# Kernel tuning notes

Measured on AMD Instinct MI355X. Metric: run time of the kernel, lower is better.

## Reference

```python
import jax, jax.numpy as jnp
import numpy as np

B, T, H, DFF = 32, 4096, 512, 512  # hidden_size=512, d_ff=512, h feature dim = 2*H


def setup_inputs() -> dict:
    key = jax.random.key(0)
    ks = jax.random.split(key, 8)
    sc = 0.02
    return {
        "s": jax.random.normal(ks[0], (B, H), dtype=jnp.float32),
        "h": jax.random.normal(ks[1], (B, T, 2 * H), dtype=jnp.float32),
        "W_a_w": jax.random.normal(ks[2], (DFF, H), dtype=jnp.float32) * sc,
        "W_a_b": jnp.zeros((DFF,), dtype=jnp.float32),
        "U_a_w": jax.random.normal(ks[3], (DFF, 2 * H), dtype=jnp.float32) * sc,
        "U_a_b": jnp.zeros((DFF,), dtype=jnp.float32),
        "V_a_w": jax.random.normal(ks[4], (1, DFF), dtype=jnp.float32) * sc,
        "V_a_b": jnp.zeros((1,), dtype=jnp.float32),
    }


def reference(s, h, W_a_w, W_a_b, U_a_w, U_a_b, V_a_w, V_a_b):
    # Bahdanau additive attention scoring (NOTE: original has no softmax).
    ws = s @ W_a_w.T + W_a_b                              # [B, d_ff]
    uh = jnp.einsum('bte,fe->btf', h, U_a_w) + U_a_b       # [B, T, d_ff]
    x = jnp.tanh(ws[:, None, :] + uh)                      # [B, T, d_ff]
    energy = x @ V_a_w[0] + V_a_b[0]                       # [B, T]
    context = jnp.einsum('bt,bte->be', energy, h)          # [B, 2*hidden]
    return context
```

## Files before the change

### kernel.cpp

```cpp
#include <hip/hip_runtime.h>
#include <cstdint>
#include <cstddef>

#define B_SZ 32
#define T_SZ 4096
#define H2   1024
#define DFF_ 512
#define TM   64
#define BK   32
#define SPH  16
#define NSTEP 32

typedef __attribute__((ext_vector_type(8))) short bf16x8;
typedef __attribute__((ext_vector_type(4))) float f32x4;

__device__ __forceinline__ unsigned short f2bf(float x) {
  unsigned u = __float_as_uint(x);
  u += 0x7fffu + ((u >> 16) & 1u);
  return (unsigned short)(u >> 16);
}

__global__ void prep_u_kernel(const float* __restrict__ U,
                              unsigned short* __restrict__ Upk) {
  int g = blockIdx.x * 256 + threadIdx.x;
  int j  = g & 7;
  int l  = (g >> 3) & 63;
  int ct = (g >> 9) & 31;
  int ks = g >> 14;
  int f  = ct * 16 + (l & 15);
  int k  = ks * 32 + (l >> 4) * 8 + j;
  Upk[g] = f2bf(U[f * H2 + k]);
}

__global__ void prep_ws_kernel(const float* __restrict__ s, const float* __restrict__ W,
                               const float* __restrict__ Wb, const float* __restrict__ Ub,
                               float* __restrict__ wsm) {
  int idx = blockIdx.x * 256 + threadIdx.x;
  int b = idx >> 9, f = idx & 511;
  const float4* s4 = (const float4*)(s + b * 512);
  const float4* w4 = (const float4*)(W + f * 512);
  float acc = 0.f;
  #pragma unroll 4
  for (int i = 0; i < 128; ++i) {
    float4 a = s4[i], w = w4[i];
    acc += a.x * w.x + a.y * w.y + a.z * w.z + a.w * w.w;
  }
  wsm[idx] = acc + Wb[f] + Ub[f];
}

__global__ __launch_bounds__(512, 4) void attn_main(
    const float* __restrict__ h, const unsigned short* __restrict__ Upk,
    const float* __restrict__ wsm, const float* __restrict__ Vw,
    const float* __restrict__ Vb, float* __restrict__ out) {
  __shared__ unsigned short As[SPH * 2048];
  __shared__ float ws_s[DFF_];
  __shared__ float V_s[DFF_];
  __shared__ float energy_part[8][TM];
  __shared__ float energy_s[TM];

  const int tid  = threadIdx.x;
  const int blk  = blockIdx.x;
  const int b    = blk >> 6;
  const int t0   = (blk & 63) * TM;
  const int lane = tid & 63;
  const int cg   = tid >> 6;
  const int ln15 = lane & 15;
  const int q4   = lane >> 4;

  ws_s[tid] = wsm[b * DFF_ + tid];
  V_s[tid]  = Vw[tid];

  const int arow = tid >> 3;
  const int ak   = (tid & 7) * 4;
  const int a_off = (arow >> 4) * 512 + (ak >> 3) * 128 + (arow & 15) * 8 + (ak & 7);
  const float* hbase = h + ((size_t)(b * T_SZ + t0)) * H2;
  const float* hrow  = hbase + (size_t)arow * H2 + ak;

  const bf16x8* Upk8 = (const bf16x8*)Upk;

  f32x4 acc[16];
  #pragma unroll
  for (int i = 0; i < 16; ++i) acc[i] = (f32x4){0.f, 0.f, 0.f, 0.f};

  for (int hk = 0; hk < 2; ++hk) {
    if (hk) __syncthreads();
    {
      float4 avv[8];
      #pragma unroll
      for (int j = 0; j < 8; ++j) avv[j] = *(const float4*)(hrow + hk * 512 + j * BK);
      #pragma unroll
      for (int j = 0; j < 8; ++j) {
        ushort4 ab;
        ab.x = f2bf(avv[j].x); ab.y = f2bf(avv[j].y);
        ab.z = f2bf(avv[j].z); ab.w = f2bf(avv[j].w);
        *(ushort4*)&As[j * 2048 + a_off] = ab;
      }
      #pragma unroll
      for (int j = 0; j < 8; ++j) avv[j] = *(const float4*)(hrow + hk * 512 + (j + 8) * BK);
      #pragma unroll
      for (int j = 0; j < 8; ++j) {
        ushort4 ab;
        ab.x = f2bf(avv[j].x); ab.y = f2bf(avv[j].y);
        ab.z = f2bf(avv[j].z); ab.w = f2bf(avv[j].w);
        *(ushort4*)&As[(j + 8) * 2048 + a_off] = ab;
      }
    }
    __syncthreads();
    const int ksbase = hk * SPH;
    bf16x8 bcur[4], bnxt[4];
    {
      size_t base = ((size_t)(ksbase * 32 + cg * 4)) * 64 + lane;
      #pragma unroll
      for (int i = 0; i < 4; ++i) bcur[i] = Upk8[base + (size_t)i * 64];
    }
    #pragma unroll
    for (int s = 0; s < SPH; ++s) {
      if (s < SPH - 1) {
        size_t base = ((size_t)((ksbase + s + 1) * 32 + cg * 4)) * 64 + lane;
        #pragma unroll
        for (int i = 0; i < 4; ++i) bnxt[i] = Upk8[base + (size_t)i * 64];
      }
      bf16x8 af[4];
      #pragma unroll
      for (int rt = 0; rt < 4; ++rt)
        af[rt] = *(const bf16x8*)&As[s * 2048 + rt * 512 + lane * 8];
      #pragma unroll
      for (int ct2 = 0; ct2 < 4; ++ct2)
        #pragma unroll
        for (int rt = 0; rt < 4; ++rt)
          acc[ct2 * 4 + rt] =
            __builtin_amdgcn_mfma_f32_16x16x32_bf16(af[rt], bcur[ct2], acc[ct2 * 4 + rt], 0, 0, 0);
      #pragma unroll
      for (int i = 0; i < 4; ++i) bcur[i] = bnxt[i];
    }
  }

  float esum[16];
  #pragma unroll
  for (int i = 0; i < 16; ++i) esum[i] = 0.f;
  #pragma unroll
  for (int ct2 = 0; ct2 < 4; ++ct2) {
    int f = cg * 64 + ct2 * 16 + ln15;
    float wsf = ws_s[f], vf = V_s[f];
    #pragma unroll
    for (int rt = 0; rt < 4; ++rt) {
      #pragma unroll
      for (int rg = 0; rg < 4; ++rg) {
        float z = wsf + acc[ct2 * 4 + rt][rg];
        float e = __expf(2.f * z);
        float x = 1.f - 2.f / (e + 1.f);
        esum[rt * 4 + rg] += x * vf;
      }
    }
  }
  #pragma unroll
  for (int i = 0; i < 16; ++i) {
    #pragma unroll
    for (int m = 1; m < 16; m <<= 1) esum[i] += __shfl_xor(esum[i], m, 64);
  }
  if (ln15 == 0) {
    #pragma unroll
    for (int rt = 0; rt < 4; ++rt)
      #pragma unroll
      for (int rg = 0; rg < 4; ++rg)
        energy_part[cg][rt * 16 + q4 * 4 + rg] = esum[rt * 4 + rg];
  }
  __syncthreads();
  if (tid < TM) {
    float e = Vb[0];
    #pragma unroll
    for (int w = 0; w < 8; ++w) e += energy_part[w][tid];
    energy_s[tid] = e;
  }
  __syncthreads();

  int e0 = tid * 2;
  float c0 = 0.f, c1 = 0.f;
  const float2* h2p = (const float2*)hbase + (e0 >> 1);
  #pragma unroll 4
  for (int row = 0; row < TM; ++row) {
    float en = energy_s[row];
    float2 hv = h2p[(size_t)row * (H2 / 2)];
    c0 += en * hv.x;
    c1 += en * hv.y;
  }
  atomicAdd(&out[b * H2 + e0], c0);
  atomicAdd(&out[b * H2 + e0 + 1], c1);
}

extern "C" void kernel_launch(void* const* d_in, const int* in_sizes, int n_in,
                              void* d_out, int out_size, void* d_ws, size_t ws_size,
                              hipStream_t stream) {
  const float* s  = (const float*)d_in[0];
  const float* h  = (const float*)d_in[1];
  const float* Ww = (const float*)d_in[2];
  const float* Wb = (const float*)d_in[3];
  const float* Uw = (const float*)d_in[4];
  const float* Ub = (const float*)d_in[5];
  const float* Vw = (const float*)d_in[6];
  const float* Vb = (const float*)d_in[7];
  float* out = (float*)d_out;

  unsigned short* Upk = (unsigned short*)d_ws;
  float* wsm = (float*)((char*)d_ws + (size_t)NSTEP * 32768);

  hipMemsetAsync(out, 0, (size_t)out_size * sizeof(float), stream);
  prep_u_kernel<<<(DFF_ * H2) / 256, 256, 0, stream>>>(Uw, Upk);
  prep_ws_kernel<<<(B_SZ * DFF_) / 256, 256, 0, stream>>>(s, Ww, Wb, Ub, wsm);
  attn_main<<<B_SZ * (T_SZ / TM), 512, 0, stream>>>(h, Upk, wsm, Vw, Vb, out);
}
```

Measured before the change: 884.6 us.

## Stream h tiles via async global-to-LDS loads with double-buffered bf16 chunks

Replaces the two large register-staged loads of the h tile with 128-column chunks fetched by global_load_lds directly into an fp32 LDS staging buffer. Each chunk is converted to bf16 in a double-buffered A tile while the next chunk's load is in flight, overlapping memory traffic with MFMA work. LDS use changes: the bf16 A buffer shrinks and an fp32 staging buffer is added, which may alter occupancy, and each chunk adds two more barriers. The context loop unroll is also raised from 4 to 8.

```diff
diff --git a/kernel.cpp b/kernel.cpp
--- a/kernel.cpp
+++ b/kernel.cpp
@@ -7,8 +7,8 @@
 #define H2   1024
 #define DFF_ 512
 #define TM   64
-#define BK   32
-#define SPH  16
+#define CH_K 128
+#define NCHUNK 8
 #define NSTEP 32
 
 typedef __attribute__((ext_vector_type(8))) short bf16x8;
@@ -18,6 +18,12 @@
   unsigned u = __float_as_uint(x);
   u += 0x7fffu + ((u >> 16) & 1u);
   return (unsigned short)(u >> 16);
+}
+
+__device__ __forceinline__ void gll16(const float* g, void* l) {
+  __builtin_amdgcn_global_load_lds(
+      (const __attribute__((address_space(1))) unsigned int*)g,
+      (__attribute__((address_space(3))) unsigned int*)l, 16, 0, 0);
 }
 
 __global__ void prep_u_kernel(const float* __restrict__ U,
@@ -52,7 +58,8 @@
     const float* __restrict__ h, const unsigned short* __restrict__ Upk,
     const float* __restrict__ wsm, const float* __restrict__ Vw,
     const float* __restrict__ Vb, float* __restrict__ out) {
-  __shared__ unsigned short As[SPH * 2048];
+  __shared__ float F32c[8320];
+  __shared__ unsigned short As16[2][4 * 2048];
   __shared__ float ws_s[DFF_];
   __shared__ float V_s[DFF_];
   __shared__ float energy_part[8][TM];
@@ -70,11 +77,15 @@
   ws_s[tid] = wsm[b * DFF_ + tid];
   V_s[tid]  = Vw[tid];
 
-  const int arow = tid >> 3;
-  const int ak   = (tid & 7) * 4;
-  const int a_off = (arow >> 4) * 512 + (ak >> 3) * 128 + (arow & 15) * 8 + (ak & 7);
   const float* hbase = h + ((size_t)(b * T_SZ + t0)) * H2;
-  const float* hrow  = hbase + (size_t)arow * H2 + ak;
+
+  const float* gA = hbase + (size_t)(8 * cg + (lane >> 5)) * H2 + (lane & 31) * 4;
+  char* lA = (char*)F32c + cg * (4 * 1040);
+
+  const int arow  = tid >> 3;
+  const int acq   = tid & 7;
+  const int rbyte = (arow >> 1) * 1040 + (arow & 1) * 512 + acq * 16;
+  const int a_off = (arow >> 4) * 512 + (acq >> 1) * 128 + (arow & 15) * 8 + (acq & 1) * 4;
 
   const bf16x8* Upk8 = (const bf16x8*)Upk;
 
@@ -82,48 +93,55 @@
   #pragma unroll
   for (int i = 0; i < 16; ++i) acc[i] = (f32x4){0.f, 0.f, 0.f, 0.f};
 
-  for (int hk = 0; hk < 2; ++hk) {
-    if (hk) __syncthreads();
-    {
-      float4 avv[8];
-      #pragma unroll
-      for (int j = 0; j < 8; ++j) avv[j] = *(const float4*)(hrow + hk * 512 + j * BK);
-      #pragma unroll
-      for (int j = 0; j < 8; ++j) {
-        ushort4 ab;
-        ab.x = f2bf(avv[j].x); ab.y = f2bf(avv[j].y);
-        ab.z = f2bf(avv[j].z); ab.w = f2bf(avv[j].w);
-        *(ushort4*)&As[j * 2048 + a_off] = ab;
-      }
-      #pragma unroll
-      for (int j = 0; j < 8; ++j) avv[j] = *(const float4*)(hrow + hk * 512 + (j + 8) * BK);
-      #pragma unroll
-      for (int j = 0; j < 8; ++j) {
-        ushort4 ab;
-        ab.x = f2bf(avv[j].x); ab.y = f2bf(avv[j].y);
-        ab.z = f2bf(avv[j].z); ab.w = f2bf(avv[j].w);
-        *(ushort4*)&As[(j + 8) * 2048 + a_off] = ab;
-      }
-    }
-    __syncthreads();
-    const int ksbase = hk * SPH;
-    bf16x8 bcur[4], bnxt[4];
-    {
-      size_t base = ((size_t)(ksbase * 32 + cg * 4)) * 64 + lane;
-      #pragma unroll
-      for (int i = 0; i < 4; ++i) bcur[i] = Upk8[base + (size_t)i * 64];
-    }
-    #pragma unroll
-    for (int s = 0; s < SPH; ++s) {
-      if (s < SPH - 1) {
-        size_t base = ((size_t)((ksbase + s + 1) * 32 + cg * 4)) * 64 + lane;
+  {
+    const float* g0 = gA;
+    gll16(g0,          lA);
+    gll16(g0 + 2 * H2, lA + 1040);
+    gll16(g0 + 4 * H2, lA + 2080);
+    gll16(g0 + 6 * H2, lA + 3120);
+  }
+  asm volatile("s_waitcnt vmcnt(0)" ::: "memory");
+  __syncthreads();
+  {
+    unsigned short* dst = &As16[0][0];
+    #pragma unroll
+    for (int j = 0; j < 4; ++j) {
+      float4 v = *(const float4*)((const char*)F32c + rbyte + j * 128);
+      ushort4 ab;
+      ab.x = f2bf(v.x); ab.y = f2bf(v.y); ab.z = f2bf(v.z); ab.w = f2bf(v.w);
+      *(ushort4*)&dst[j * 2048 + a_off] = ab;
+    }
+  }
+  __syncthreads();
+  {
+    const float* g0 = gA + CH_K;
+    gll16(g0,          lA);
+    gll16(g0 + 2 * H2, lA + 1040);
+    gll16(g0 + 4 * H2, lA + 2080);
+    gll16(g0 + 6 * H2, lA + 3120);
+  }
+
+  bf16x8 bcur[4], bnxt[4];
+  {
+    int ub = (cg * 4) * 64 + lane;
+    #pragma unroll
+    for (int i = 0; i < 4; ++i) bcur[i] = Upk8[ub + i * 64];
+  }
+
+  for (int c2 = 0; c2 < NCHUNK; ++c2) {
+    const unsigned short* Ab = &As16[c2 & 1][0];
+    #pragma unroll
+    for (int sl = 0; sl < 4; ++sl) {
+      if (sl < 3 || c2 < NCHUNK - 1) {
+        int sgn = c2 * 4 + sl + 1;
+        int ub = (sgn * 32 + cg * 4) * 64 + lane;
         #pragma unroll
-        for (int i = 0; i < 4; ++i) bnxt[i] = Upk8[base + (size_t)i * 64];
+        for (int i = 0; i < 4; ++i) bnxt[i] = Upk8[ub + i * 64];
       }
       bf16x8 af[4];
       #pragma unroll
       for (int rt = 0; rt < 4; ++rt)
-        af[rt] = *(const bf16x8*)&As[s * 2048 + rt * 512 + lane * 8];
+        af[rt] = *(const bf16x8*)&Ab[sl * 2048 + rt * 512 + lane * 8];
       #pragma unroll
       for (int ct2 = 0; ct2 < 4; ++ct2)
         #pragma unroll
@@ -133,6 +151,26 @@
       #pragma unroll
       for (int i = 0; i < 4; ++i) bcur[i] = bnxt[i];
     }
+    if (c2 < NCHUNK - 1) {
+      asm volatile("s_waitcnt vmcnt(0)" ::: "memory");
+      __syncthreads();
+      unsigned short* dst = &As16[(c2 + 1) & 1][0];
+      #pragma unroll
+      for (int j = 0; j < 4; ++j) {
+        float4 v = *(const float4*)((const char*)F32c + rbyte + j * 128);
+        ushort4 ab;
+        ab.x = f2bf(v.x); ab.y = f2bf(v.y); ab.z = f2bf(v.z); ab.w = f2bf(v.w);
+        *(ushort4*)&dst[j * 2048 + a_off] = ab;
+      }
+      __syncthreads();
+      if (c2 < NCHUNK - 2) {
+        const float* g0 = gA + (c2 + 2) * CH_K;
+        gll16(g0,          lA);
+        gll16(g0 + 2 * H2, lA + 1040);
+        gll16(g0 + 4 * H2, lA + 2080);
+        gll16(g0 + 6 * H2, lA + 3120);
+      }
+    }
   }
 
   float esum[16];
@@ -177,7 +215,7 @@
   int e0 = tid * 2;
   float c0 = 0.f, c1 = 0.f;
   const float2* h2p = (const float2*)hbase + (e0 >> 1);
-  #pragma unroll 4
+  #pragma unroll 8
   for (int row = 0; row < TM; ++row) {
     float en = energy_s[row];
     float2 hv = h2p[(size_t)row * (H2 / 2)];
```

New measurement: 848.1 us. 4.1% less time.

## Warp-specialize attention kernel with async global-to-LDS h loader pipeline

Applied to the files above, without the earlier changes.

Adds two producer waves per block that stream h tiles straight into LDS with global_load_lds into a triple-buffered fp32 ring. They convert each tile to bf16 into a double-buffered operand buffer while the eight consumer waves run MFMA on the previous chunk. The goal is to hide h load latency and the conversion work behind the matrix math, where before everything ran in two serialized load-then-compute phases. The cost is a larger LDS footprint (about 128KB for the fp32 ring plus the bf16 buffers), a launch bound of 640 threads with 3 blocks per CU, and hand-written waitcnt and barrier bookkeeping that is fragile.

```diff
diff --git a/kernel.cpp b/kernel.cpp
--- a/kernel.cpp
+++ b/kernel.cpp
@@ -7,8 +7,7 @@
 #define H2   1024
 #define DFF_ 512
 #define TM   64
-#define BK   32
-#define SPH  16
+#define NCHUNK 8
 #define NSTEP 32
 
 typedef __attribute__((ext_vector_type(8))) short bf16x8;
@@ -18,6 +17,44 @@
   unsigned u = __float_as_uint(x);
   u += 0x7fffu + ((u >> 16) & 1u);
   return (unsigned short)(u >> 16);
+}
+
+__device__ __forceinline__ void gll16(const float* g, void* l) {
+  __builtin_amdgcn_global_load_lds(
+      (const __attribute__((address_space(1))) unsigned int*)g,
+      (__attribute__((address_space(3))) unsigned int*)l, 16, 0, 0);
+}
+
+__device__ __forceinline__ void blk_barrier() {
+  asm volatile("" ::: "memory");
+  __builtin_amdgcn_s_barrier();
+  asm volatile("" ::: "memory");
+}
+
+__device__ __forceinline__ void issue_chunk(int p, int lane, const float* hbase,
+                                            int c, char* slotbase) {
+  char* lb = slotbase + p * 16384;
+  const float* gb = hbase + (size_t)(p * 32 + (lane >> 5)) * H2 + c * 128 + (lane & 31) * 4;
+  #pragma unroll
+  for (int u = 0; u < 16; ++u)
+    gll16(gb + (size_t)(2 * u) * H2, lb + u * 1024);
+}
+
+__device__ __forceinline__ void convert_chunk(int p, int lane, const float* slot,
+                                              unsigned short* dst) {
+  const int v = p * 64 + lane;
+  const int arow = v >> 1;
+  const int half = v & 1;
+  #pragma unroll
+  for (int m = 0; m < 16; ++m) {
+    int qq = half * 16 + ((m + arow) & 15);
+    float4 x = *(const float4*)&slot[arow * 128 + qq * 4];
+    ushort4 ab;
+    ab.x = f2bf(x.x); ab.y = f2bf(x.y); ab.z = f2bf(x.z); ab.w = f2bf(x.w);
+    int woff = (qq >> 3) * 2048 + (arow >> 4) * 512 + ((qq & 7) >> 1) * 128
+             + (arow & 15) * 8 + (qq & 1) * 4;
+    *(ushort4*)&dst[woff] = ab;
+  }
 }
 
 __global__ void prep_u_kernel(const float* __restrict__ U,
@@ -48,11 +85,12 @@
   wsm[idx] = acc + Wb[f] + Ub[f];
 }
 
-__global__ __launch_bounds__(512, 4) void attn_main(
+__global__ __launch_bounds__(640, 3) void attn_main(
     const float* __restrict__ h, const unsigned short* __restrict__ Upk,
     const float* __restrict__ wsm, const float* __restrict__ Vw,
     const float* __restrict__ Vb, float* __restrict__ out) {
-  __shared__ unsigned short As[SPH * 2048];
+  __shared__ float F32c[3][8192];
+  __shared__ unsigned short As16[2][8192];
   __shared__ float ws_s[DFF_];
   __shared__ float V_s[DFF_];
   __shared__ float energy_part[8][TM];
@@ -63,107 +101,104 @@
   const int b    = blk >> 6;
   const int t0   = (blk & 63) * TM;
   const int lane = tid & 63;
-  const int cg   = tid >> 6;
+  const int wave = tid >> 6;
   const int ln15 = lane & 15;
   const int q4   = lane >> 4;
 
-  ws_s[tid] = wsm[b * DFF_ + tid];
-  V_s[tid]  = Vw[tid];
-
-  const int arow = tid >> 3;
-  const int ak   = (tid & 7) * 4;
-  const int a_off = (arow >> 4) * 512 + (ak >> 3) * 128 + (arow & 15) * 8 + (ak & 7);
   const float* hbase = h + ((size_t)(b * T_SZ + t0)) * H2;
-  const float* hrow  = hbase + (size_t)arow * H2 + ak;
-
   const bf16x8* Upk8 = (const bf16x8*)Upk;
 
   f32x4 acc[16];
   #pragma unroll
   for (int i = 0; i < 16; ++i) acc[i] = (f32x4){0.f, 0.f, 0.f, 0.f};
-
-  for (int hk = 0; hk < 2; ++hk) {
-    if (hk) __syncthreads();
-    {
-      float4 avv[8];
-      #pragma unroll
-      for (int j = 0; j < 8; ++j) avv[j] = *(const float4*)(hrow + hk * 512 + j * BK);
-      #pragma unroll
-      for (int j = 0; j < 8; ++j) {
-        ushort4 ab;
-        ab.x = f2bf(avv[j].x); ab.y = f2bf(avv[j].y);
-        ab.z = f2bf(avv[j].z); ab.w = f2bf(avv[j].w);
-        *(ushort4*)&As[j * 2048 + a_off] = ab;
+  bf16x8 bcur[4], bnxt[4];
+
+  if (wave < 8) {
+    ws_s[tid] = wsm[b * DFF_ + tid];
+    V_s[tid]  = Vw[tid];
+    int ub = (wave * 4) * 64 + lane;
+    #pragma unroll
+    for (int i = 0; i < 4; ++i) bcur[i] = Upk8[ub + i * 64];
+  } else {
+    const int p = wave - 8;
+    issue_chunk(p, lane, hbase, 0, (char*)F32c[0]);
+    issue_chunk(p, lane, hbase, 1, (char*)F32c[1]);
+    issue_chunk(p, lane, hbase, 2, (char*)F32c[2]);
+    asm volatile("s_waitcnt vmcnt(32)" ::: "memory");
+    convert_chunk(p, lane, F32c[0], As16[0]);
+    asm volatile("s_waitcnt lgkmcnt(0)" ::: "memory");
+  }
+  blk_barrier();
+
+  for (int c = 0; c < NCHUNK; ++c) {
+    if (wave < 8) {
+      const unsigned short* Ab = As16[c & 1];
+      #pragma unroll
+      for (int sl = 0; sl < 4; ++sl) {
+        int g = c * 4 + sl;
+        if (g < NSTEP - 1) {
+          int ub = ((g + 1) * 32 + wave * 4) * 64 + lane;
+          #pragma unroll
+          for (int i = 0; i < 4; ++i) bnxt[i] = Upk8[ub + i * 64];
+        }
+        bf16x8 af[4];
+        #pragma unroll
+        for (int rt = 0; rt < 4; ++rt)
+          af[rt] = *(const bf16x8*)&Ab[sl * 2048 + rt * 512 + lane * 8];
+        #pragma unroll
+        for (int ct2 = 0; ct2 < 4; ++ct2)
+          #pragma unroll
+          for (int rt = 0; rt < 4; ++rt)
+            acc[ct2 * 4 + rt] =
+              __builtin_amdgcn_mfma_f32_16x16x32_bf16(af[rt], bcur[ct2], acc[ct2 * 4 + rt], 0, 0, 0);
+        #pragma unroll
+        for (int i = 0; i < 4; ++i) bcur[i] = bnxt[i];
       }
-      #pragma unroll
-      for (int j = 0; j < 8; ++j) avv[j] = *(const float4*)(hrow + hk * 512 + (j + 8) * BK);
-      #pragma unroll
-      for (int j = 0; j < 8; ++j) {
-        ushort4 ab;
-        ab.x = f2bf(avv[j].x); ab.y = f2bf(avv[j].y);
-        ab.z = f2bf(avv[j].z); ab.w = f2bf(avv[j].w);
-        *(ushort4*)&As[(j + 8) * 2048 + a_off] = ab;
+    } else {
+      const int p = wave - 8;
+      if (c < NCHUNK - 1) {
+        if (c < NCHUNK - 2) asm volatile("s_waitcnt vmcnt(16)" ::: "memory");
+        else                asm volatile("s_waitcnt vmcnt(0)"  ::: "memory");
+        convert_chunk(p, lane, F32c[(c + 1) % 3], As16[(c + 1) & 1]);
+        if (c < NCHUNK - 3)
+          issue_chunk(p, lane, hbase, c + 3, (char*)F32c[(c + 3) % 3]);
+        asm volatile("s_waitcnt lgkmcnt(0)" ::: "memory");
       }
     }
-    __syncthreads();
-    const int ksbase = hk * SPH;
-    bf16x8 bcur[4], bnxt[4];
-    {
-      size_t base = ((size_t)(ksbase * 32 + cg * 4)) * 64 + lane;
-      #pragma unroll
-      for (int i = 0; i < 4; ++i) bcur[i] = Upk8[base + (size_t)i * 64];
-    }
-    #pragma unroll
-    for (int s = 0; s < SPH; ++s) {
-      if (s < SPH - 1) {
-        size_t base = ((size_t)((ksbase + s + 1) * 32 + cg * 4)) * 64 + lane;
-        #pragma unroll
-        for (int i = 0; i < 4; ++i) bnxt[i] = Upk8[base + (size_t)i * 64];
+    blk_barrier();
+  }
+
+  if (wave < 8) {
+    float esum[16];
+    #pragma unroll
+    for (int i = 0; i < 16; ++i) esum[i] = 0.f;
+    #pragma unroll
+    for (int ct2 = 0; ct2 < 4; ++ct2) {
+      int f = wave * 64 + ct2 * 16 + ln15;
+      float wsf = ws_s[f], vf = V_s[f];
+      #pragma unroll
+      for (int rt = 0; rt < 4; ++rt) {
+        #pragma unroll
+        for (int rg = 0; rg < 4; ++rg) {
+          float z = wsf + acc[ct2 * 4 + rt][rg];
+          float e = __expf(2.f * z);
+          float x = 1.f - 2.f / (e + 1.f);
+          esum[rt * 4 + rg] += x * vf;
+        }
       }
-      bf16x8 af[4];
+    }
+    #pragma unroll
+    for (int i = 0; i < 16; ++i) {
+      #pragma unroll
+      for (int m = 1; m < 16; m <<= 1) esum[i] += __shfl_xor(esum[i], m, 64);
+    }
+    if (ln15 == 0) {
       #pragma unroll
       for (int rt = 0; rt < 4; ++rt)
-        af[rt] = *(const bf16x8*)&As[s * 2048 + rt * 512 + lane * 8];
-      #pragma unroll
-      for (int ct2 = 0; ct2 < 4; ++ct2)
-        #pragma unroll
-        for (int rt = 0; rt < 4; ++rt)
-          acc[ct2 * 4 + rt] =
-            __builtin_amdgcn_mfma_f32_16x16x32_bf16(af[rt], bcur[ct2], acc[ct2 * 4 + rt], 0, 0, 0);
-      #pragma unroll
-      for (int i = 0; i < 4; ++i) bcur[i] = bnxt[i];
-    }
-  }
-
-  float esum[16];
-  #pragma unroll
-  for (int i = 0; i < 16; ++i) esum[i] = 0.f;
-  #pragma unroll
-  for (int ct2 = 0; ct2 < 4; ++ct2) {
-    int f = cg * 64 + ct2 * 16 + ln15;
-    float wsf = ws_s[f], vf = V_s[f];
-    #pragma unroll
-    for (int rt = 0; rt < 4; ++rt) {
-      #pragma unroll
-      for (int rg = 0; rg < 4; ++rg) {
-        float z = wsf + acc[ct2 * 4 + rt][rg];
-        float e = __expf(2.f * z);
-        float x = 1.f - 2.f / (e + 1.f);
-        esum[rt * 4 + rg] += x * vf;
-      }
-    }
-  }
-  #pragma unroll
-  for (int i = 0; i < 16; ++i) {
-    #pragma unroll
-    for (int m = 1; m < 16; m <<= 1) esum[i] += __shfl_xor(esum[i], m, 64);
-  }
-  if (ln15 == 0) {
-    #pragma unroll
-    for (int rt = 0; rt < 4; ++rt)
-      #pragma unroll
-      for (int rg = 0; rg < 4; ++rg)
-        energy_part[cg][rt * 16 + q4 * 4 + rg] = esum[rt * 4 + rg];
+        #pragma unroll
+        for (int rg = 0; rg < 4; ++rg)
+          energy_part[wave][rt * 16 + q4 * 4 + rg] = esum[rt * 4 + rg];
+    }
   }
   __syncthreads();
   if (tid < TM) {
@@ -174,18 +209,20 @@
   }
   __syncthreads();
 
-  int e0 = tid * 2;
-  float c0 = 0.f, c1 = 0.f;
-  const float2* h2p = (const float2*)hbase + (e0 >> 1);
-  #pragma unroll 4
-  for (int row = 0; row < TM; ++row) {
-    float en = energy_s[row];
-    float2 hv = h2p[(size_t)row * (H2 / 2)];
-    c0 += en * hv.x;
-    c1 += en * hv.y;
-  }
-  atomicAdd(&out[b * H2 + e0], c0);
-  atomicAdd(&out[b * H2 + e0 + 1], c1);
+  if (tid < 512) {
+    int e0 = tid * 2;
+    float c0 = 0.f, c1 = 0.f;
+    const float2* h2p = (const float2*)hbase + (e0 >> 1);
+    #pragma unroll 8
+    for (int row = 0; row < TM; ++row) {
+      float en = energy_s[row];
+      float2 hv = h2p[(size_t)row * (H2 / 2)];
+      c0 += en * hv.x;
+      c1 += en * hv.y;
+    }
+    atomicAdd(&out[b * H2 + e0], c0);
+    atomicAdd(&out[b * H2 + e0 + 1], c1);
+  }
 }
 
 extern "C" void kernel_launch(void* const* d_in, const int* in_sizes, int n_in,
@@ -207,5 +244,5 @@
   hipMemsetAsync(out, 0, (size_t)out_size * sizeof(float), stream);
   prep_u_kernel<<<(DFF_ * H2) / 256, 256, 0, stream>>>(Uw, Upk);
   prep_ws_kernel<<<(B_SZ * DFF_) / 256, 256, 0, stream>>>(s, Ww, Wb, Ub, wsm);
-  attn_main<<<B_SZ * (T_SZ / TM), 512, 0, stream>>>(h, Upk, wsm, Vw, Vb, out);
-}
+  attn_main<<<B_SZ * (T_SZ / TM), 640, 0, stream>>>(h, Upk, wsm, Vw, Vb, out);
+}
```

New measurement: 981.7 us. +11.0%, slower.

## Stream h tiles via global_load_lds double-buffering overlapped with MFMA

Applied to the files above, without the earlier changes.

Replaces the two-phase load of h (register loads converted to bf16 into a large LDS buffer) with a double-buffered pipeline. Each 64-column chunk of fp32 h is fetched straight into LDS with global_load_lds, then converted into a small bf16 LDS tile while MFMAs run on the previous chunk. This shrinks LDS use and is meant to overlap global memory latency with compute. The cost is hand-written waitcnt and barrier logic that is fragile, with a barrier every chunk. The context loop unroll also goes from 4 to 8.

```diff
diff --git a/kernel.cpp b/kernel.cpp
--- a/kernel.cpp
+++ b/kernel.cpp
@@ -7,17 +7,31 @@
 #define H2   1024
 #define DFF_ 512
 #define TM   64
-#define BK   32
-#define SPH  16
+#define NCHUNK 16
 #define NSTEP 32
 
 typedef __attribute__((ext_vector_type(8))) short bf16x8;
 typedef __attribute__((ext_vector_type(4))) float f32x4;
+typedef __attribute__((ext_vector_type(8))) unsigned short u16x8;
 
 __device__ __forceinline__ unsigned short f2bf(float x) {
   unsigned u = __float_as_uint(x);
   u += 0x7fffu + ((u >> 16) & 1u);
   return (unsigned short)(u >> 16);
+}
+
+__device__ __forceinline__ void gll16(const float* g, void* l) {
+  __builtin_amdgcn_global_load_lds(
+      (const __attribute__((address_space(1))) unsigned int*)g,
+      (__attribute__((address_space(3))) unsigned int*)l, 16, 0, 0);
+}
+
+__device__ __forceinline__ void memfence_sched() { asm volatile("" ::: "memory"); }
+
+__device__ __forceinline__ void blk_barrier() {
+  asm volatile("" ::: "memory");
+  __builtin_amdgcn_s_barrier();
+  asm volatile("" ::: "memory");
 }
 
 __global__ void prep_u_kernel(const float* __restrict__ U,
@@ -52,7 +66,8 @@
     const float* __restrict__ h, const unsigned short* __restrict__ Upk,
     const float* __restrict__ wsm, const float* __restrict__ Vw,
     const float* __restrict__ Vb, float* __restrict__ out) {
-  __shared__ unsigned short As[SPH * 2048];
+  __shared__ float F32c[2][4096];
+  __shared__ unsigned short As16[2][4096];
   __shared__ float ws_s[DFF_];
   __shared__ float V_s[DFF_];
   __shared__ float energy_part[8][TM];
@@ -63,76 +78,93 @@
   const int b    = blk >> 6;
   const int t0   = (blk & 63) * TM;
   const int lane = tid & 63;
-  const int cg   = tid >> 6;
+  const int wave = tid >> 6;
   const int ln15 = lane & 15;
   const int q4   = lane >> 4;
 
   ws_s[tid] = wsm[b * DFF_ + tid];
   V_s[tid]  = Vw[tid];
 
-  const int arow = tid >> 3;
-  const int ak   = (tid & 7) * 4;
-  const int a_off = (arow >> 4) * 512 + (ak >> 3) * 128 + (arow & 15) * 8 + (ak & 7);
   const float* hbase = h + ((size_t)(b * T_SZ + t0)) * H2;
-  const float* hrow  = hbase + (size_t)arow * H2 + ak;
+
+  const float* gsrc = hbase + (size_t)(8 * wave + (lane >> 4)) * H2 + (lane & 15) * 4;
+
+  const int crow = 8 * wave + (lane >> 3);
+  const int ckg  = lane & 7;
+  const int cread  = crow * 64 + ckg * 8;
+  const int cwrite = (ckg >> 2) * 2048 + (crow >> 4) * 512
+                   + ((ckg & 3) * 16 + (crow & 15)) * 8;
 
   const bf16x8* Upk8 = (const bf16x8*)Upk;
 
   f32x4 acc[16];
   #pragma unroll
   for (int i = 0; i < 16; ++i) acc[i] = (f32x4){0.f, 0.f, 0.f, 0.f};
-
-  for (int hk = 0; hk < 2; ++hk) {
-    if (hk) __syncthreads();
-    {
-      float4 avv[8];
-      #pragma unroll
-      for (int j = 0; j < 8; ++j) avv[j] = *(const float4*)(hrow + hk * 512 + j * BK);
-      #pragma unroll
-      for (int j = 0; j < 8; ++j) {
-        ushort4 ab;
-        ab.x = f2bf(avv[j].x); ab.y = f2bf(avv[j].y);
-        ab.z = f2bf(avv[j].z); ab.w = f2bf(avv[j].w);
-        *(ushort4*)&As[j * 2048 + a_off] = ab;
-      }
-      #pragma unroll
-      for (int j = 0; j < 8; ++j) avv[j] = *(const float4*)(hrow + hk * 512 + (j + 8) * BK);
-      #pragma unroll
-      for (int j = 0; j < 8; ++j) {
-        ushort4 ab;
-        ab.x = f2bf(avv[j].x); ab.y = f2bf(avv[j].y);
-        ab.z = f2bf(avv[j].z); ab.w = f2bf(avv[j].w);
-        *(ushort4*)&As[(j + 8) * 2048 + a_off] = ab;
+  bf16x8 bcur[8];
+
+  gll16(gsrc,            (char*)&F32c[0][0] + wave * 2048);
+  gll16(gsrc + 4 * H2,   (char*)&F32c[0][0] + wave * 2048 + 1024);
+  memfence_sched();
+  #pragma unroll
+  for (int st = 0; st < 2; ++st)
+    #pragma unroll
+    for (int i = 0; i < 4; ++i)
+      bcur[st * 4 + i] = Upk8[(size_t)(st * 32 + wave * 4 + i) * 64 + lane];
+  memfence_sched();
+  gll16(gsrc + 64,          (char*)&F32c[1][0] + wave * 2048);
+  gll16(gsrc + 64 + 4 * H2, (char*)&F32c[1][0] + wave * 2048 + 1024);
+  asm volatile("s_waitcnt vmcnt(10)" ::: "memory");
+  {
+    const float* src = &F32c[0][cread];
+    float4 x0 = *(const float4*)src;
+    float4 x1 = *(const float4*)(src + 4);
+    u16x8 o;
+    o[0] = f2bf(x0.x); o[1] = f2bf(x0.y); o[2] = f2bf(x0.z); o[3] = f2bf(x0.w);
+    o[4] = f2bf(x1.x); o[5] = f2bf(x1.y); o[6] = f2bf(x1.z); o[7] = f2bf(x1.w);
+    *(u16x8*)&As16[0][cwrite] = o;
+  }
+  blk_barrier();
+
+  for (int c = 0; c < NCHUNK; ++c) {
+    const unsigned short* Ab = &As16[c & 1][0];
+    #pragma unroll
+    for (int st = 0; st < 2; ++st) {
+      #pragma unroll
+      for (int rt = 0; rt < 4; ++rt) {
+        bf16x8 af = *(const bf16x8*)&Ab[st * 2048 + rt * 512 + lane * 8];
+        #pragma unroll
+        for (int ct2 = 0; ct2 < 4; ++ct2)
+          acc[ct2 * 4 + rt] =
+            __builtin_amdgcn_mfma_f32_16x16x32_bf16(af, bcur[st * 4 + ct2],
+                                                    acc[ct2 * 4 + rt], 0, 0, 0);
       }
     }
-    __syncthreads();
-    const int ksbase = hk * SPH;
-    bf16x8 bcur[4], bnxt[4];
-    {
-      size_t base = ((size_t)(ksbase * 32 + cg * 4)) * 64 + lane;
-      #pragma unroll
-      for (int i = 0; i < 4; ++i) bcur[i] = Upk8[base + (size_t)i * 64];
+    if (c < NCHUNK - 1) {
+      asm volatile("s_waitcnt vmcnt(0)" ::: "memory");
+      {
+        const float* src = &F32c[(c + 1) & 1][cread];
+        float4 x0 = *(const float4*)src;
+        float4 x1 = *(const float4*)(src + 4);
+        u16x8 o;
+        o[0] = f2bf(x0.x); o[1] = f2bf(x0.y); o[2] = f2bf(x0.z); o[3] = f2bf(x0.w);
+        o[4] = f2bf(x1.x); o[5] = f2bf(x1.y); o[6] = f2bf(x1.z); o[7] = f2bf(x1.w);
+        *(u16x8*)&As16[(c + 1) & 1][cwrite] = o;
+      }
+      blk_barrier();
+      const int g0 = (c + 1) * 2;
+      #pragma unroll
+      for (int st = 0; st < 2; ++st)
+        #pragma unroll
+        for (int i = 0; i < 4; ++i)
+          bcur[st * 4 + i] = Upk8[(size_t)((g0 + st) * 32 + wave * 4 + i) * 64 + lane];
+      memfence_sched();
+      if (c < NCHUNK - 2) {
+        const float* gs = gsrc + (c + 2) * 64;
+        char* ld = (char*)&F32c[c & 1][0] + wave * 2048;
+        gll16(gs,          ld);
+        gll16(gs + 4 * H2, ld + 1024);
+      }
     }
-    #pragma unroll
-    for (int s = 0; s < SPH; ++s) {
-      if (s < SPH - 1) {
-        size_t base = ((size_t)((ksbase + s + 1) * 32 + cg * 4)) * 64 + lane;
-        #pragma unroll
-        for (int i = 0; i < 4; ++i) bnxt[i] = Upk8[base + (size_t)i * 64];
-      }
-      bf16x8 af[4];
-      #pragma unroll
-      for (int rt = 0; rt < 4; ++rt)
-        af[rt] = *(const bf16x8*)&As[s * 2048 + rt * 512 + lane * 8];
-      #pragma unroll
-      for (int ct2 = 0; ct2 < 4; ++ct2)
-        #pragma unroll
-        for (int rt = 0; rt < 4; ++rt)
-          acc[ct2 * 4 + rt] =
-            __builtin_amdgcn_mfma_f32_16x16x32_bf16(af[rt], bcur[ct2], acc[ct2 * 4 + rt], 0, 0, 0);
-      #pragma unroll
-      for (int i = 0; i < 4; ++i) bcur[i] = bnxt[i];
-    }
   }
 
   float esum[16];
@@ -140,7 +172,7 @@
   for (int i = 0; i < 16; ++i) esum[i] = 0.f;
   #pragma unroll
   for (int ct2 = 0; ct2 < 4; ++ct2) {
-    int f = cg * 64 + ct2 * 16 + ln15;
+    int f = wave * 64 + ct2 * 16 + ln15;
     float wsf = ws_s[f], vf = V_s[f];
     #pragma unroll
     for (int rt = 0; rt < 4; ++rt) {
@@ -163,7 +195,7 @@
     for (int rt = 0; rt < 4; ++rt)
       #pragma unroll
       for (int rg = 0; rg < 4; ++rg)
-        energy_part[cg][rt * 16 + q4 * 4 + rg] = esum[rt * 4 + rg];
+        energy_part[wave][rt * 16 + q4 * 4 + rg] = esum[rt * 4 + rg];
   }
   __syncthreads();
   if (tid < TM) {
@@ -177,7 +209,7 @@
   int e0 = tid * 2;
   float c0 = 0.f, c1 = 0.f;
   const float2* h2p = (const float2*)hbase + (e0 >> 1);
-  #pragma unroll 4
+  #pragma unroll 8
   for (int row = 0; row < TM; ++row) {
     float en = energy_s[row];
     float2 hv = h2p[(size_t)row * (H2 / 2)];
```

New measurement: 866.5 us. 1.02x faster.
